# Kernel optimization log

Measured on AMD Instinct MI355X. Metric: run time of the kernel, lower is better.

Reference implementation:

```python
import jax, jax.numpy as jnp
import numpy as np

N = 100000     # nodes
E = 1600000    # edges
H = 64         # hidden_channels
FIN = 4        # input feature dim (GraphNorm(4))
EPS = 1e-5
STEPS = 3      # Set2Set processing steps


def setup_inputs() -> dict:
    key = jax.random.key(0)
    ks = jax.random.split(key, 20)
    rn = lambda k, shape, s=1.0: jax.random.normal(k, shape, dtype=jnp.float32) * s

    def gn_params(k, d):
        k1, k2 = jax.random.split(k)
        return (1.0 + 0.1 * rn(k1, (d,)), 0.1 * rn(k2, (d,)), jnp.ones((d,), jnp.float32))

    inp = {}
    inp['x'] = rn(ks[0], (N, FIN))
    inp['gn0_w'], inp['gn0_b'], inp['gn0_ms'] = gn_params(ks[1], FIN)
    inp['W1'] = rn(ks[2], (FIN, H), 1.0 / np.sqrt(FIN))
    inp['b1'] = 0.01 * rn(ks[3], (H,))
    inp['a1'] = 0.25 * jnp.ones((H,), jnp.float32)
    inp['gn1_w'], inp['gn1_b'], inp['gn1_ms'] = gn_params(ks[4], H)
    inp['W2'] = rn(ks[5], (H, H), 1.0 / np.sqrt(H))
    inp['b2'] = 0.01 * rn(ks[6], (H,))
    inp['a2'] = 0.25 * jnp.ones((H,), jnp.float32)
    inp['gn2_w'], inp['gn2_b'], inp['gn2_ms'] = gn_params(ks[7], H)
    inp['W3'] = rn(ks[8], (H, H), 1.0 / np.sqrt(H))
    inp['b3'] = 0.01 * rn(ks[9], (H,))
    inp['gn3_w'], inp['gn3_b'], inp['gn3_ms'] = gn_params(ks[10], H)
    s = 1.0 / np.sqrt(H)
    inp['Wih'] = rn(ks[11], (4 * H, 2 * H), s)  # LSTM input weights, gate order i,f,g,o
    inp['Whh'] = rn(ks[12], (4 * H, H), s)
    inp['bih'] = rn(ks[13], (4 * H,), s)
    inp['bhh'] = rn(ks[14], (4 * H,), s)
    inp['edge_index'] = jax.random.randint(ks[15], (2, E), 0, N, dtype=jnp.int32)
    return inp


def _graph_norm(x, w, b, ms):
    # single graph (batch all zeros): per-feature mean/var over all nodes
    mean = x.mean(0)
    out = x - ms * mean
    var = (out * out).mean(0)
    return w * out / jnp.sqrt(var + EPS) + b


def _prelu(x, a):
    return jnp.where(x >= 0, x, a * x)


def _gcn(x, W, b, src, dst, dinv):
    # GCNConv: D^{-1/2} (A + I) D^{-1/2} X W + b
    xw = x @ W
    coef = dinv[src] * dinv[dst]
    agg = jax.ops.segment_sum(xw[src] * coef[:, None], dst, num_segments=N)
    agg = agg + xw * (dinv * dinv)[:, None]  # self-loop contribution
    return agg + b


def reference(x, gn0_w, gn0_b, gn0_ms, W1, b1, a1, gn1_w, gn1_b, gn1_ms,
              W2, b2, a2, gn2_w, gn2_b, gn2_ms, W3, b3, gn3_w, gn3_b, gn3_ms,
              Wih, Whh, bih, bhh, edge_index):
    src, dst = edge_index[0], edge_index[1]
    deg = jax.ops.segment_sum(jnp.ones((E,), jnp.float32), dst, num_segments=N) + 1.0
    dinv = 1.0 / jnp.sqrt(deg)

    h = _graph_norm(x, gn0_w, gn0_b, gn0_ms)
    h = _prelu(_gcn(h, W1, b1, src, dst, dinv), a1)
    h = _graph_norm(h, gn1_w, gn1_b, gn1_ms)
    h = _prelu(_gcn(h, W2, b2, src, dst, dinv), a2)
    h = _graph_norm(h, gn2_w, gn2_b, gn2_ms)
    h = _gcn(h, W3, b3, src, dst, dinv)
    h = _graph_norm(h, gn3_w, gn3_b, gn3_ms)

    # Set2Set pooling over a single graph (batch forced to zeros in forward)
    q_star = jnp.zeros((1, 2 * H), jnp.float32)
    hs = jnp.zeros((1, H), jnp.float32)
    c = jnp.zeros((1, H), jnp.float32)
    for _ in range(STEPS):
        gates = q_star @ Wih.T + bih + hs @ Whh.T + bhh
        i, f, g, o = jnp.split(gates, 4, axis=-1)
        c = jax.nn.sigmoid(f) * c + jax.nn.sigmoid(i) * jnp.tanh(g)
        hs = jax.nn.sigmoid(o) * jnp.tanh(c)
        e = h @ hs[0]                    # [N] attention logits
        a = jax.nn.softmax(e)
        r = (a[:, None] * h).sum(0, keepdims=True)  # [1, H] readout
        q_star = jnp.concatenate([hs, r], axis=-1)
    return q_star  # [1, 2H]
```

## Files before the change

kernel.cpp:

```cpp
#include <hip/hip_runtime.h>

#define NN 100000
#define NE 1600000
#define HID 64
#define EPSV 1e-5f
#define NB_ATT 512
#define NGRP 12500

#define NBUK 391
#define BCAP 4608
#define BTILE 2048
#define NTILES 782

#define SM_SUMS(l)  ((l)*128)
#define SM_SUMSQ(l) ((l)*128 + 64)
#define SM_HS       512
#define SM_C        576
#define SM_HV       768
#define SM_EOFF     832
#define SM_GCUR     1024
#define SM_ZEND     1424
#define SM_GPART    1424

#define NPAD        100352L
#define OFF_DINV    7684L
#define OFF_H       (OFF_DINV + NPAD)
#define OFF_Y32     (OFF_H + 6400000L)
#define OFF_PART    (OFF_Y32 + 3200000L)
#define OFF_INT     (OFF_PART + 69632L)

static __device__ __forceinline__ unsigned bf16rne(float f) {
  unsigned u = __float_as_uint(f);
  return (u + 0x7fffu + ((u >> 16) & 1u)) >> 16;
}
static __device__ __forceinline__ unsigned packbf2(float lo, float hi) {
  return bf16rne(lo) | (bf16rne(hi) << 16);
}
static __device__ __forceinline__ float bflo(unsigned w) { return __uint_as_float(w << 16); }
static __device__ __forceinline__ float bfhi(unsigned w) { return __uint_as_float(w & 0xffff0000u); }

static __device__ __forceinline__ void gn_affine(int j, const float* w, const float* b,
                                                 const float* ms, const float* sums,
                                                 const float* sumsq, float& sc, float& sh) {
  const float invn = 1.0f / (float)NN;
  float mean = sums[j] * invn;
  float ex2  = sumsq[j] * invn;
  float m    = ms[j];
  float var  = ex2 - m * mean * mean * (2.0f - m);
  sc = w[j] * rsqrtf(var + EPSV);
  sh = b[j] - sc * m * mean;
}

__global__ __launch_bounds__(256) void k_bin(const int* __restrict__ src, const int* __restrict__ dst,
                                             const float* __restrict__ x,
                                             int* __restrict__ gcursor, unsigned* __restrict__ stage,
                                             float* __restrict__ gpart) {
  __shared__ int hist[NBUK], base[NBUK];
  __shared__ float gred[4][8];
  int t = threadIdx.x, lane = t & 63, w = t >> 6;
  long tile0 = (long)blockIdx.x * BTILE;
  for (int b = t; b < NBUK; b += 256) hist[b] = 0;
  __syncthreads();
  unsigned v[8]; int bk[8];
#pragma unroll
  for (int k = 0; k < 8; ++k) {
    long e = tile0 + k * 256 + t;
    if (e < NE) {
      int d = dst[e], s = src[e];
      bk[k] = d >> 8;
      v[k] = ((unsigned)(d & 255) << 24) | (unsigned)s;
      atomicAdd(&hist[bk[k]], 1);
    } else bk[k] = -1;
  }
  __syncthreads();
  for (int b = t; b < NBUK; b += 256) {
    int c = hist[b];
    base[b] = c ? atomicAdd(&gcursor[b], c) : 0;
    hist[b] = 0;
  }
  __syncthreads();
#pragma unroll
  for (int k = 0; k < 8; ++k) {
    if (bk[k] >= 0) {
      int bkk = bk[k];
      int off = atomicAdd(&hist[bkk], 1);
      stage[(long)bkk * BCAP + base[bkk] + off] = v[k];
    }
  }
  const float4* x4 = (const float4*)x;
  float4 s4 = make_float4(0.f, 0.f, 0.f, 0.f);
  float4 q4 = make_float4(0.f, 0.f, 0.f, 0.f);
  int stride = gridDim.x * 256;
  for (int i = blockIdx.x * 256 + t; i < NN; i += stride) {
    float4 xv = x4[i];
    s4.x += xv.x; s4.y += xv.y; s4.z += xv.z; s4.w += xv.w;
    q4.x += xv.x * xv.x; q4.y += xv.y * xv.y; q4.z += xv.z * xv.z; q4.w += xv.w * xv.w;
  }
#pragma unroll
  for (int off = 32; off; off >>= 1) {
    s4.x += __shfl_xor(s4.x, off, 64); s4.y += __shfl_xor(s4.y, off, 64);
    s4.z += __shfl_xor(s4.z, off, 64); s4.w += __shfl_xor(s4.w, off, 64);
    q4.x += __shfl_xor(q4.x, off, 64); q4.y += __shfl_xor(q4.y, off, 64);
    q4.z += __shfl_xor(q4.z, off, 64); q4.w += __shfl_xor(q4.w, off, 64);
  }
  if (lane == 0) {
    gred[w][0] = s4.x; gred[w][1] = s4.y; gred[w][2] = s4.z; gred[w][3] = s4.w;
    gred[w][4] = q4.x; gred[w][5] = q4.y; gred[w][6] = q4.z; gred[w][7] = q4.w;
  }
  __syncthreads();
  if (t < 8) gpart[blockIdx.x * 8 + t] = gred[0][t] + gred[1][t] + gred[2][t] + gred[3][t];
}

__global__ __launch_bounds__(512) void k_bscan(const int* __restrict__ gcursor,
                                               int* __restrict__ boff, int* __restrict__ rowptr,
                                               const float* __restrict__ gpart,
                                               float* __restrict__ sums0, float* __restrict__ sumsq0) {
  __shared__ int ws[8];
  __shared__ float gl[64][8];
  int t = threadIdx.x, lane = t & 63;
  int c = (t < NBUK) ? gcursor[t] : 0;
  int incl = c;
#pragma unroll
  for (int off = 1; off < 64; off <<= 1) {
    int u = __shfl_up(incl, off, 64);
    if (lane >= off) incl += u;
  }
  if (lane == 63) ws[t >> 6] = incl;
  __syncthreads();
  if (t == 0) {
    int s = 0;
#pragma unroll
    for (int w = 0; w < 8; ++w) { int tv = ws[w]; ws[w] = s; s += tv; }
  }
  __syncthreads();
  if (t < NBUK) boff[t] = incl - c + ws[t >> 6];
  if (t == 0) { boff[NBUK] = NE; rowptr[NN] = NE; }
  float acc = 0.f;
  int f = t & 7, r = t >> 3;
  for (int i = r; i < NTILES; i += 64) acc += gpart[i * 8 + f];
  gl[r][f] = acc;
  __syncthreads();
  if (t < 8) {
    float s = 0.f;
#pragma unroll 16
    for (int rr = 0; rr < 64; ++rr) s += gl[rr][t];
    if (t < 4) sums0[t] = s;
    else sumsq0[t - 4] = s;
  }
}

__global__ __launch_bounds__(256) void k_bsort(const unsigned* __restrict__ stage,
                                               const int* __restrict__ boff,
                                               int* __restrict__ col, int* __restrict__ rowptr,
                                               float* __restrict__ dinv) {
  __shared__ int hist[256], cur[256];
  __shared__ int ws[4];
  int b = blockIdx.x;
  int t = threadIdx.x, lane = t & 63;
  long sb = (long)b * BCAP;
  int b0 = boff[b], cb = boff[b + 1] - b0;
  hist[t] = 0;
  __syncthreads();
  for (int j = t; j < cb; j += 256)
    atomicAdd(&hist[stage[sb + j] >> 24], 1);
  __syncthreads();
  int c = hist[t];
  int incl = c;
#pragma unroll
  for (int off = 1; off < 64; off <<= 1) {
    int u = __shfl_up(incl, off, 64);
    if (lane >= off) incl += u;
  }
  if (lane == 63) ws[t >> 6] = incl;
  __syncthreads();
  int woff = 0;
  if (t >= 64) woff += ws[0];
  if (t >= 128) woff += ws[1];
  if (t >= 192) woff += ws[2];
  int gbase = b0 + (incl - c) + woff;
  int node = b * 256 + t;
  if (node < NN) {
    rowptr[node] = gbase;
    dinv[node] = rsqrtf((float)c + 1.0f);
  }
  cur[t] = gbase;
  __syncthreads();
  for (int j = t; j < cb; j += 256) {
    unsigned v = stage[sb + j];
    int pos = atomicAdd(&cur[v >> 24], 1);
    col[pos] = (int)(v & 0xffffffu);
  }
}

template <int D>
__global__ __launch_bounds__(256) void k_mm(const float* __restrict__ hin, const float* __restrict__ W,
                                            const float* __restrict__ gw, const float* __restrict__ gb,
                                            const float* __restrict__ gms,
                                            const float* __restrict__ sums, const float* __restrict__ sumsq,
                                            const float* __restrict__ dinv,
                                            unsigned* __restrict__ y32) {
  __shared__ float4 Ws4[D][16];
  __shared__ float4 woff4[16];
  __shared__ float scale[D], shift[D];
  __shared__ float hl[16][68];
  int t = threadIdx.x;
  if (t < D) {
    float sc, sh;
    gn_affine(t, gw, gb, gms, sums, sumsq, sc, sh);
    scale[t] = sc; shift[t] = sh;
  }
  __syncthreads();
  for (int idx = t; idx < D * 64; idx += 256) {
    int k = idx >> 6;
    ((float*)Ws4)[idx] = scale[k] * W[idx];
  }
  __syncthreads();
  if (t < 64) {
    float o = 0.f;
#pragma unroll
    for (int k = 0; k < D; ++k) o += shift[k] * W[k * 64 + t];
    ((float*)woff4)[t] = o;
  }
  __syncthreads();

  int row = t >> 4, cg = t & 15;
  const int nG = NN / 16;
  for (int g = blockIdx.x; g < nG; g += gridDim.x) {
    if (D == 64) {
      *(float4*)&hl[row][cg * 4] = *(const float4*)(hin + (long)(g * 16 + row) * 64 + cg * 4);
    } else {
      if (t < 64) hl[t >> 2][t & 3] = hin[g * 64 + t];
    }
    __syncthreads();
    float4 acc = woff4[cg];
#pragma unroll
    for (int k = 0; k < D; ++k) {
      float hk = hl[row][k];
      float4 w4 = Ws4[k][cg];
      acc.x += hk * w4.x; acc.y += hk * w4.y;
      acc.z += hk * w4.z; acc.w += hk * w4.w;
    }
    int node = g * 16 + row;
    float di = dinv[node];
    uint2 u;
    u.x = packbf2(di * acc.x, di * acc.y);
    u.y = packbf2(di * acc.z, di * acc.w);
    *(uint2*)(y32 + ((long)(cg >> 1) * NN + node) * 4 + (cg & 1) * 2) = u;
    __syncthreads();
  }
}

#define ACCW(WV) { f[0]+=bflo(WV.x); f[1]+=bfhi(WV.x); f[2]+=bflo(WV.y); f[3]+=bfhi(WV.y); \
                   f[4]+=bflo(WV.z); f[5]+=bfhi(WV.z); f[6]+=bflo(WV.w); f[7]+=bfhi(WV.w); }

template <bool PR, bool HB>
__global__ __launch_bounds__(256) void k_gather_fin(const uint4* __restrict__ y4x,
                                                    const int* __restrict__ rowptr, const int* __restrict__ col,
                                                    const float* __restrict__ dinv,
                                                    const float* __restrict__ b, const float* __restrict__ a,
                                                    float* __restrict__ h, uint4* __restrict__ hb4,
                                                    float* __restrict__ sums, float* __restrict__ sumsq) {
  __shared__ float ssum[8], ssq[8];
  int t = threadIdx.x, lane = t & 63, w = t >> 6;
  int n = lane >> 3, j = lane & 7;
  int s = blockIdx.x & 7;
  const uint4* yp = y4x + (long)s * NN;
  if (t < 8) { ssum[t] = 0.f; ssq[t] = 0.f; }
  __syncthreads();
  float bv[8], av[8];
#pragma unroll
  for (int k = 0; k < 8; ++k) {
    bv[k] = b[8 * s + k];
    av[k] = PR ? a[8 * s + k] : 1.f;
  }
  float sa[8] = {0,0,0,0,0,0,0,0}, qa[8] = {0,0,0,0,0,0,0,0};
  int gstride = (gridDim.x >> 3) * 4;
  for (int g = (blockIdx.x >> 3) * 4 + w; g < NGRP; g += gstride) {
    int i0 = g * 8;
    int r = (lane < 9) ? rowptr[i0 + lane] : 0;
    int p0 = __shfl(r, n, 64);
    int p1 = __shfl(r, n + 1, 64);
    float f[8] = {0,0,0,0,0,0,0,0};
    for (int p = p0 + j; p < p1; p += 8) {
      int c = col[p];
      uint4 wv = yp[c];
      ACCW(wv);
    }
    if (((p1 - p0) & 7) == j) {
      uint4 wv = yp[i0 + n];
      ACCW(wv);
    }
#pragma unroll
    for (int k = 0; k < 8; ++k) {
      float v = f[k];
      v += __shfl_xor(v, 1, 64);
      v += __shfl_xor(v, 2, 64);
      v += __shfl_xor(v, 4, 64);
      f[k] = v;
    }
    if (j == 0) {
      int i = i0 + n;
      float di = dinv[i];
      float vo[8];
#pragma unroll
      for (int k = 0; k < 8; ++k) {
        float v = di * f[k] + bv[k];
        if (PR && v < 0.f) v *= av[k];
        vo[k] = v;
        sa[k] += v; qa[k] += v * v;
      }
      if (HB) {
        uint4 u;
        u.x = packbf2(vo[0], vo[1]); u.y = packbf2(vo[2], vo[3]);
        u.z = packbf2(vo[4], vo[5]); u.w = packbf2(vo[6], vo[7]);
        hb4[(long)i * 8 + s] = u;
      } else {
        *(float4*)(h + (long)i * 64 + 8 * s)     = make_float4(vo[0], vo[1], vo[2], vo[3]);
        *(float4*)(h + (long)i * 64 + 8 * s + 4) = make_float4(vo[4], vo[5], vo[6], vo[7]);
      }
    }
  }
  if (j == 0) {
#pragma unroll
    for (int k = 0; k < 8; ++k) { atomicAdd(&ssum[k], sa[k]); atomicAdd(&ssq[k], qa[k]); }
  }
  __syncthreads();
  if (t < 8) {
    atomicAdd(&sums[8 * s + t], ssum[t]);
    atomicAdd(&sumsq[8 * s + t], ssq[t]);
  }
}

__global__ __launch_bounds__(256) void k_att(const uint4* __restrict__ hb4, const float* __restrict__ sm,
                                             float* __restrict__ part) {
  __shared__ float gm[32], gz[32], gr[32][64];
  int t = threadIdx.x;
  int grp = t >> 3, l7 = t & 7;
  float hvr[8];
#pragma unroll
  for (int k = 0; k < 8; ++k) hvr[k] = sm[SM_HV + 8 * l7 + k];
  float eoff = sm[SM_EOFF];
  float m = -3.4e38f, z = 0.f;
  float r[8] = {0,0,0,0,0,0,0,0};
  int ngrp = gridDim.x * 32;
  for (int i = blockIdx.x * 32 + grp; i < NN; i += ngrp) {
    uint4 hw = hb4[(long)i * 8 + l7];
    float hx[8] = { bflo(hw.x), bfhi(hw.x), bflo(hw.y), bfhi(hw.y),
                    bflo(hw.z), bfhi(hw.z), bflo(hw.w), bfhi(hw.w) };
    float dot = 0.f;
#pragma unroll
    for (int k = 0; k < 8; ++k) dot += hx[k] * hvr[k];
    dot += __shfl_xor(dot, 1, 64);
    dot += __shfl_xor(dot, 2, 64);
    dot += __shfl_xor(dot, 4, 64);
    float e = dot + eoff;
    float mn = fmaxf(m, e);
    float sc = expf(m - mn);
    float pb = expf(e - mn);
    z = z * sc + pb;
#pragma unroll
    for (int k = 0; k < 8; ++k) r[k] = r[k] * sc + pb * hx[k];
    m = mn;
  }
#pragma unroll
  for (int k = 0; k < 8; ++k) gr[grp][8 * l7 + k] = r[k];
  if (l7 == 0) { gm[grp] = m; gz[grp] = z; }
  __syncthreads();
  if (t < 64) {
    float mb = gm[0];
#pragma unroll
    for (int k = 1; k < 32; ++k) mb = fmaxf(mb, gm[k]);
    float rb = 0.f, zb = 0.f;
#pragma unroll 8
    for (int k = 0; k < 32; ++k) {
      float scl = expf(gm[k] - mb);
      rb += gr[k][t] * scl;
      zb += gz[k] * scl;
    }
    part[blockIdx.x * 68 + t] = rb;
    if (t == 0) { part[blockIdx.x * 68 + 64] = mb; part[blockIdx.x * 68 + 65] = zb; }
  }
}

__global__ __launch_bounds__(256) void k_attfin(const float* __restrict__ part,
                                                const float* __restrict__ gw, const float* __restrict__ gb,
                                                const float* __restrict__ gms,
                                                const float* __restrict__ sums, const float* __restrict__ sumsq,
                                                const float* __restrict__ Wih, const float* __restrict__ Whh,
                                                const float* __restrict__ bih, const float* __restrict__ bhh,
                                                float* __restrict__ sm, float* __restrict__ out, int mode) {
  __shared__ float hsL[64], cL[64], qsL[128], gL[256], red[256], sf[NB_ATT], rr4[4][64];
  int t = threadIdx.x, lane = t & 63, w = t >> 6;
  if (t < 64) { hsL[t] = sm[SM_HS + t]; cL[t] = sm[SM_C + t]; }
  __syncthreads();
  if (mode > 0) {
    float mv0 = part[t * 68 + 64];
    float mv1 = part[(t + 256) * 68 + 64];
    red[t] = fmaxf(mv0, mv1); __syncthreads();
    for (int s = 128; s; s >>= 1) { if (t < s) red[t] = fmaxf(red[t], red[t + s]); __syncthreads(); }
    float mg = red[0];
    __syncthreads();
    float sc0 = expf(mv0 - mg), sc1 = expf(mv1 - mg);
    sf[t] = sc0; sf[t + 256] = sc1;
    red[t] = part[t * 68 + 65] * sc0 + part[(t + 256) * 68 + 65] * sc1;
    __syncthreads();
    for (int s = 128; s; s >>= 1) { if (t < s) red[t] += red[t + s]; __syncthreads(); }
    float zg = red[0];
    __syncthreads();
    float racc = 0.f;
#pragma unroll 8
    for (int jx = 0; jx < 128; ++jx) {
      int bk = 4 * jx + w;
      racc += part[bk * 68 + lane] * sf[bk];
    }
    rr4[w][lane] = racc;
    __syncthreads();
    if (t < 64) {
      float rg = rr4[0][t] + rr4[1][t] + rr4[2][t] + rr4[3][t];
      float sc, sh;
      gn_affine(t, gw, gb, gms, sums, sumsq, sc, sh);
      float rr = sc * (rg / zg) + sh;
      qsL[t] = hsL[t]; qsL[64 + t] = rr;
      if (mode == 2) { out[t] = hsL[t]; out[64 + t] = rr; }
    }
  } else {
    if (t < 64) { qsL[t] = 0.f; qsL[64 + t] = 0.f; hsL[t] = 0.f; cL[t] = 0.f; }
  }
  __syncthreads();
  if (mode == 2) return;
  float g = bih[t] + bhh[t];
#pragma unroll 16
  for (int k = 0; k < 128; ++k) g += qsL[k] * Wih[t * 128 + k];
#pragma unroll 16
  for (int k = 0; k < 64; ++k) g += hsL[k] * Whh[t * 64 + k];
  gL[t] = g;
  __syncthreads();
  if (t < 64) {
    float ig = 1.f / (1.f + expf(-gL[t]));
    float fg = 1.f / (1.f + expf(-gL[64 + t]));
    float gg = tanhf(gL[128 + t]);
    float og = 1.f / (1.f + expf(-gL[192 + t]));
    float c = fg * cL[t] + ig * gg;
    float hsn = og * tanhf(c);
    sm[SM_C + t] = c;
    sm[SM_HS + t] = hsn;
    float sc, sh;
    gn_affine(t, gw, gb, gms, sums, sumsq, sc, sh);
    sm[SM_HV + t] = sc * hsn;
    red[t] = sh * hsn;
  }
  __syncthreads();
  if (t == 0) {
    float s = 0.f;
    for (int k = 0; k < 64; ++k) s += red[k];
    sm[SM_EOFF] = s;
  }
}

extern "C" void kernel_launch(void* const* d_in, const int* in_sizes, int n_in,
                              void* d_out, int out_size, void* d_ws, size_t ws_size,
                              hipStream_t stream) {
  const float* x     = (const float*)d_in[0];
  const float* gn0_w = (const float*)d_in[1];
  const float* gn0_b = (const float*)d_in[2];
  const float* gn0_ms= (const float*)d_in[3];
  const float* W1    = (const float*)d_in[4];
  const float* b1    = (const float*)d_in[5];
  const float* a1    = (const float*)d_in[6];
  const float* gn1_w = (const float*)d_in[7];
  const float* gn1_b = (const float*)d_in[8];
  const float* gn1_ms= (const float*)d_in[9];
  const float* W2    = (const float*)d_in[10];
  const float* b2    = (const float*)d_in[11];
  const float* a2    = (const float*)d_in[12];
  const float* gn2_w = (const float*)d_in[13];
  const float* gn2_b = (const float*)d_in[14];
  const float* gn2_ms= (const float*)d_in[15];
  const float* W3    = (const float*)d_in[16];
  const float* b3    = (const float*)d_in[17];
  const float* gn3_w = (const float*)d_in[18];
  const float* gn3_b = (const float*)d_in[19];
  const float* gn3_ms= (const float*)d_in[20];
  const float* Wih   = (const float*)d_in[21];
  const float* Whh   = (const float*)d_in[22];
  const float* bih   = (const float*)d_in[23];
  const float* bhh   = (const float*)d_in[24];
  const int*   eidx  = (const int*)d_in[25];
  const int* esrc = eidx;
  const int* edst = eidx + NE;

  float* sm   = (float*)d_ws;
  int* gcursor= (int*)(sm + SM_GCUR);
  float* gpart= sm + SM_GPART;
  float* dinv = sm + OFF_DINV;
  float* h    = sm + OFF_H;
  unsigned* stage = (unsigned*)(sm + OFF_H);
  uint4* hb4  = (uint4*)(sm + OFF_H);
  unsigned* y32 = (unsigned*)(sm + OFF_Y32);
  const uint4* y4 = (const uint4*)y32;
  float* part = sm + OFF_PART;
  int* col    = (int*)(sm + OFF_INT);
  int* rowptr = col + NE;
  int* boff   = rowptr + NPAD;
  float* out  = (float*)d_out;

  hipMemsetAsync(sm, 0, SM_ZEND * sizeof(float), stream);

  k_bin<<<NTILES, 256, 0, stream>>>(esrc, edst, x, gcursor, stage, gpart);
  k_bscan<<<1, 512, 0, stream>>>(gcursor, boff, rowptr, gpart,
                                 sm + SM_SUMS(0), sm + SM_SUMSQ(0));
  k_bsort<<<NBUK, 256, 0, stream>>>(stage, boff, col, rowptr, dinv);

  k_mm<4><<<1024, 256, 0, stream>>>(x, W1, gn0_w, gn0_b, gn0_ms,
                                    sm + SM_SUMS(0), sm + SM_SUMSQ(0), dinv, y32);
  k_gather_fin<true, false><<<2048, 256, 0, stream>>>(y4, rowptr, col, dinv, b1, a1, h, nullptr,
                                                      sm + SM_SUMS(1), sm + SM_SUMSQ(1));
  k_mm<64><<<1024, 256, 0, stream>>>(h, W2, gn1_w, gn1_b, gn1_ms,
                                     sm + SM_SUMS(1), sm + SM_SUMSQ(1), dinv, y32);
  k_gather_fin<true, false><<<2048, 256, 0, stream>>>(y4, rowptr, col, dinv, b2, a2, h, nullptr,
                                                      sm + SM_SUMS(2), sm + SM_SUMSQ(2));
  k_mm<64><<<1024, 256, 0, stream>>>(h, W3, gn2_w, gn2_b, gn2_ms,
                                     sm + SM_SUMS(2), sm + SM_SUMSQ(2), dinv, y32);
  k_gather_fin<false, true><<<2048, 256, 0, stream>>>(y4, rowptr, col, dinv, b3, nullptr, nullptr, hb4,
                                                      sm + SM_SUMS(3), sm + SM_SUMSQ(3));

  k_attfin<<<1, 256, 0, stream>>>(part, gn3_w, gn3_b, gn3_ms,
                                  sm + SM_SUMS(3), sm + SM_SUMSQ(3),
                                  Wih, Whh, bih, bhh, sm, nullptr, 0);
  for (int s = 0; s < 3; ++s) {
    k_att<<<NB_ATT, 256, 0, stream>>>(hb4, sm, part);
    k_attfin<<<1, 256, 0, stream>>>(part, gn3_w, gn3_b, gn3_ms,
                                    sm + SM_SUMS(3), sm + SM_SUMSQ(3),
                                    Wih, Whh, bih, bhh, sm,
                                    (s == 2) ? out : nullptr, (s == 2) ? 2 : 1);
  }
}
```

Measured before the change: 433.1 us.

## Switch node features to feature-slice-major layout and prefetch rowptr in gather

Stores the gathered hidden features (fp32 and bf16) in a slice-major layout [slice][node][8] instead of node-major, and updates the transform and attention kernels to read that layout. The gather loop prefetches the next group's rowptr and unrolls the neighbor loop by two for more outstanding loads. The attention kernel is rewritten so each thread owns one node and one slice, combining per-slice dot products through shared memory with a double buffer. The intent is coalesced, contiguous per-slice reads. The cost is a __syncthreads in every attention iteration.

```diff
diff --git a/kernel.cpp b/kernel.cpp
--- a/kernel.cpp
+++ b/kernel.cpp
@@ -226,8 +226,10 @@
   int row = t >> 4, cg = t & 15;
   const int nG = NN / 16;
   for (int g = blockIdx.x; g < nG; g += gridDim.x) {
+    int node = g * 16 + row;
     if (D == 64) {
-      *(float4*)&hl[row][cg * 4] = *(const float4*)(hin + (long)(g * 16 + row) * 64 + cg * 4);
+      *(float4*)&hl[row][cg * 4] =
+        *(const float4*)(hin + ((long)(cg >> 1) * NN + node) * 8 + (cg & 1) * 4);
     } else {
       if (t < 64) hl[t >> 2][t & 3] = hin[g * 64 + t];
     }
@@ -240,7 +242,6 @@
       acc.x += hk * w4.x; acc.y += hk * w4.y;
       acc.z += hk * w4.z; acc.w += hk * w4.w;
     }
-    int node = g * 16 + row;
     float di = dinv[node];
     uint2 u;
     u.x = packbf2(di * acc.x, di * acc.y);
@@ -258,7 +259,7 @@
                                                     const int* __restrict__ rowptr, const int* __restrict__ col,
                                                     const float* __restrict__ dinv,
                                                     const float* __restrict__ b, const float* __restrict__ a,
-                                                    float* __restrict__ h, uint4* __restrict__ hb4,
+                                                    float* __restrict__ hp, uint4* __restrict__ hb4p,
                                                     float* __restrict__ sums, float* __restrict__ sumsq) {
   __shared__ float ssum[8], ssq[8];
   int t = threadIdx.x, lane = t & 63, w = t >> 6;
@@ -275,20 +276,31 @@
   }
   float sa[8] = {0,0,0,0,0,0,0,0}, qa[8] = {0,0,0,0,0,0,0,0};
   int gstride = (gridDim.x >> 3) * 4;
-  for (int g = (blockIdx.x >> 3) * 4 + w; g < NGRP; g += gstride) {
+  int g = (blockIdx.x >> 3) * 4 + w;
+  int rcur = 0;
+  if (g < NGRP && lane < 9) rcur = rowptr[g * 8 + lane];
+  while (g < NGRP) {
+    int gn = g + gstride;
+    int rn = 0;
+    if (gn < NGRP && lane < 9) rn = rowptr[gn * 8 + lane];
     int i0 = g * 8;
-    int r = (lane < 9) ? rowptr[i0 + lane] : 0;
-    int p0 = __shfl(r, n, 64);
-    int p1 = __shfl(r, n + 1, 64);
+    int p0 = __shfl(rcur, n, 64);
+    int p1 = __shfl(rcur, n + 1, 64);
     float f[8] = {0,0,0,0,0,0,0,0};
-    for (int p = p0 + j; p < p1; p += 8) {
-      int c = col[p];
-      uint4 wv = yp[c];
-      ACCW(wv);
+    int p = p0 + j;
+    for (; p + 8 < p1; p += 16) {
+      int c0 = col[p], c1 = col[p + 8];
+      uint4 wa = yp[c0];
+      uint4 wb = yp[c1];
+      ACCW(wa); ACCW(wb);
+    }
+    if (p < p1) {
+      uint4 wa = yp[col[p]];
+      ACCW(wa);
     }
     if (((p1 - p0) & 7) == j) {
-      uint4 wv = yp[i0 + n];
-      ACCW(wv);
+      uint4 wa = yp[i0 + n];
+      ACCW(wa);
     }
 #pragma unroll
     for (int k = 0; k < 8; ++k) {
@@ -313,12 +325,14 @@
         uint4 u;
         u.x = packbf2(vo[0], vo[1]); u.y = packbf2(vo[2], vo[3]);
         u.z = packbf2(vo[4], vo[5]); u.w = packbf2(vo[6], vo[7]);
-        hb4[(long)i * 8 + s] = u;
+        hb4p[(long)s * NN + i] = u;
       } else {
-        *(float4*)(h + (long)i * 64 + 8 * s)     = make_float4(vo[0], vo[1], vo[2], vo[3]);
-        *(float4*)(h + (long)i * 64 + 8 * s + 4) = make_float4(vo[4], vo[5], vo[6], vo[7]);
+        float* hd = hp + ((long)s * NN + i) * 8;
+        *(float4*)hd       = make_float4(vo[0], vo[1], vo[2], vo[3]);
+        *(float4*)(hd + 4) = make_float4(vo[4], vo[5], vo[6], vo[7]);
       }
     }
+    g = gn; rcur = rn;
   }
   if (j == 0) {
 #pragma unroll
@@ -331,29 +345,34 @@
   }
 }
 
-__global__ __launch_bounds__(256) void k_att(const uint4* __restrict__ hb4, const float* __restrict__ sm,
+__global__ __launch_bounds__(256) void k_att(const uint4* __restrict__ hb4p, const float* __restrict__ sm,
                                              float* __restrict__ part) {
-  __shared__ float gm[32], gz[32], gr[32][64];
+  __shared__ float ldot[2][8][32];
+  __shared__ float lr[8][32][8];
+  __shared__ float lz[32];
   int t = threadIdx.x;
-  int grp = t >> 3, l7 = t & 7;
+  int p = t >> 5, nn = t & 31;
   float hvr[8];
 #pragma unroll
-  for (int k = 0; k < 8; ++k) hvr[k] = sm[SM_HV + 8 * l7 + k];
+  for (int k = 0; k < 8; ++k) hvr[k] = sm[SM_HV + 8 * p + k];
   float eoff = sm[SM_EOFF];
   float m = -3.4e38f, z = 0.f;
   float r[8] = {0,0,0,0,0,0,0,0};
-  int ngrp = gridDim.x * 32;
-  for (int i = blockIdx.x * 32 + grp; i < NN; i += ngrp) {
-    uint4 hw = hb4[(long)i * 8 + l7];
+  int buf = 0;
+  int stride = gridDim.x * 32;
+  for (int i0 = blockIdx.x * 32; i0 < NN; i0 += stride) {
+    int i = i0 + nn;
+    uint4 hw = hb4p[(long)p * NN + i];
     float hx[8] = { bflo(hw.x), bfhi(hw.x), bflo(hw.y), bfhi(hw.y),
                     bflo(hw.z), bfhi(hw.z), bflo(hw.w), bfhi(hw.w) };
-    float dot = 0.f;
-#pragma unroll
-    for (int k = 0; k < 8; ++k) dot += hx[k] * hvr[k];
-    dot += __shfl_xor(dot, 1, 64);
-    dot += __shfl_xor(dot, 2, 64);
-    dot += __shfl_xor(dot, 4, 64);
-    float e = dot + eoff;
+    float d = 0.f;
+#pragma unroll
+    for (int k = 0; k < 8; ++k) d += hx[k] * hvr[k];
+    ldot[buf][p][nn] = d;
+    __syncthreads();
+    float e = eoff;
+#pragma unroll
+    for (int pp = 0; pp < 8; ++pp) e += ldot[buf][pp][nn];
     float mn = fmaxf(m, e);
     float sc = expf(m - mn);
     float pb = expf(e - mn);
@@ -361,24 +380,29 @@
 #pragma unroll
     for (int k = 0; k < 8; ++k) r[k] = r[k] * sc + pb * hx[k];
     m = mn;
-  }
-#pragma unroll
-  for (int k = 0; k < 8; ++k) gr[grp][8 * l7 + k] = r[k];
-  if (l7 == 0) { gm[grp] = m; gz[grp] = z; }
+    buf ^= 1;
+  }
+  float mb = m;
+#pragma unroll
+  for (int off = 16; off; off >>= 1) mb = fmaxf(mb, __shfl_xor(mb, off, 64));
+  float scl = expf(m - mb);
+#pragma unroll
+  for (int k = 0; k < 8; ++k) lr[p][nn][k] = r[k] * scl;
+  if (p == 0) lz[nn] = z * scl;
   __syncthreads();
   if (t < 64) {
-    float mb = gm[0];
-#pragma unroll
-    for (int k = 1; k < 32; ++k) mb = fmaxf(mb, gm[k]);
-    float rb = 0.f, zb = 0.f;
+    int pp = t >> 3, k = t & 7;
+    float rb = 0.f;
 #pragma unroll 8
-    for (int k = 0; k < 32; ++k) {
-      float scl = expf(gm[k] - mb);
-      rb += gr[k][t] * scl;
-      zb += gz[k] * scl;
-    }
+    for (int n2 = 0; n2 < 32; ++n2) rb += lr[pp][n2][k];
     part[blockIdx.x * 68 + t] = rb;
-    if (t == 0) { part[blockIdx.x * 68 + 64] = mb; part[blockIdx.x * 68 + 65] = zb; }
+  }
+  if (t == 0) {
+    float zb = 0.f;
+#pragma unroll 8
+    for (int n2 = 0; n2 < 32; ++n2) zb += lz[n2];
+    part[blockIdx.x * 68 + 64] = mb;
+    part[blockIdx.x * 68 + 65] = zb;
   }
 }
 
```

Result: faster. 419.4 us (-3.2%).
